# Performance work log

Hardware: AMD Instinct MI355X
Metric: run time of the kernel (lower is better)

## Reference

```python
import jax, jax.numpy as jnp
import numpy as np

N_NODES = 50000
N_EDGES = 1600000
IN_FEATS = 256
ENC_H = 20
DEC_H = 64
BIAS = 0.0  # forward arg default
TEMPERATURE = 1.0


def setup_inputs() -> dict:
    key = jax.random.key(0)
    ks = jax.random.split(key, 8)
    x = jax.random.normal(ks[0], (N_NODES, IN_FEATS), dtype=jnp.float32)
    edge_index = jax.random.randint(ks[1], (2, N_EDGES), 0, N_NODES, dtype=jnp.int64)
    node_id = 42
    # GCNConv params (glorot-ish scale)
    W_gcn = jax.random.normal(ks[2], (IN_FEATS, ENC_H), dtype=jnp.float32) / np.sqrt(IN_FEATS)
    b_gcn = jnp.zeros((ENC_H,), dtype=jnp.float32)
    # decoder MLP params
    W1 = jax.random.normal(ks[3], (3 * ENC_H, DEC_H), dtype=jnp.float32) / np.sqrt(3 * ENC_H)
    b1 = jnp.zeros((DEC_H,), dtype=jnp.float32)
    W2 = jax.random.normal(ks[4], (DEC_H, 1), dtype=jnp.float32) / np.sqrt(DEC_H)
    b2 = jnp.zeros((1,), dtype=jnp.float32)
    return {"x": x, "edge_index": edge_index, "node_id": node_id,
            "W_gcn": W_gcn, "b_gcn": b_gcn, "W1": W1, "b1": b1, "W2": W2, "b2": b2}


def _gcn_conv(x, edge_index, W, b):
    """PyG GCNConv: add self loops, symmetric normalization, sum aggregation."""
    n = x.shape[0]
    xw = x @ W  # [N, ENC_H]
    loop = jnp.arange(n, dtype=edge_index.dtype)
    row = jnp.concatenate([edge_index[0], loop])  # source
    col = jnp.concatenate([edge_index[1], loop])  # target
    ones = jnp.ones(row.shape[0], dtype=x.dtype)
    deg = jax.ops.segment_sum(ones, col, num_segments=n)
    dinv = jnp.where(deg > 0, jax.lax.rsqrt(jnp.maximum(deg, 1e-12)), 0.0)
    norm = dinv[row] * dinv[col]  # [E+N]
    msgs = xw[row] * norm[:, None]
    out = jax.ops.segment_sum(msgs, col, num_segments=n)
    return out + b


def reference(x, edge_index, node_id, W_gcn, b_gcn, W1, b1, W2, b2):
    # encoder: GCN + ReLU
    enc = jax.nn.relu(_gcn_conv(x, edge_index, W_gcn, b_gcn))  # [N, ENC_H]
    # edge representation: [row_embed | col_embed | node_embed]
    rows, cols = edge_index[0], edge_index[1]
    node_embed = jnp.broadcast_to(enc[node_id], (rows.shape[0], enc.shape[1]))
    z = jnp.concatenate([enc[rows], enc[cols], node_embed], axis=1)  # [E, 3*ENC_H]
    # decoder MLP
    h = jax.nn.relu(z @ W1 + b1)
    out_dec = h @ W2 + b2  # [E, 1]
    # Gumbel-sigmoid sampling (training=True path)
    bias = BIAS + 0.0001
    u = jax.random.uniform(jax.random.key(123), out_dec.shape, dtype=out_dec.dtype)
    eps = (bias - (1.0 - bias)) * u + (1.0 - bias)  # in (bias, 1-bias)
    gate = jnp.log(eps) - jnp.log1p(-eps)
    return jax.nn.sigmoid((gate + out_dec) / TEMPERATURE)
```

## Files before the change

kernel.cpp:

```cpp
#include <hip/hip_runtime.h>
#include <hip/hip_bf16.h>

#define IN_FEATS 256
#define ENC_H    20
#define DEC_H    64
#define EPB      8192

__device__ __forceinline__ unsigned int rotl32(unsigned int x, int d) {
  return (x << d) | (x >> (32 - d));
}

__device__ __forceinline__ void threefry2x32(unsigned int k0, unsigned int k1,
                                             unsigned int x0, unsigned int x1,
                                             unsigned int& o0, unsigned int& o1) {
  unsigned int ks0 = k0, ks1 = k1, ks2 = k0 ^ k1 ^ 0x1BD11BDAu;
  x0 += ks0; x1 += ks1;
  x0 += x1; x1 = rotl32(x1, 13); x1 ^= x0;
  x0 += x1; x1 = rotl32(x1, 15); x1 ^= x0;
  x0 += x1; x1 = rotl32(x1, 26); x1 ^= x0;
  x0 += x1; x1 = rotl32(x1,  6); x1 ^= x0;
  x0 += ks1; x1 += ks2 + 1u;
  x0 += x1; x1 = rotl32(x1, 17); x1 ^= x0;
  x0 += x1; x1 = rotl32(x1, 29); x1 ^= x0;
  x0 += x1; x1 = rotl32(x1, 16); x1 ^= x0;
  x0 += x1; x1 = rotl32(x1, 24); x1 ^= x0;
  x0 += ks2; x1 += ks0 + 2u;
  x0 += x1; x1 = rotl32(x1, 13); x1 ^= x0;
  x0 += x1; x1 = rotl32(x1, 15); x1 ^= x0;
  x0 += x1; x1 = rotl32(x1, 26); x1 ^= x0;
  x0 += x1; x1 = rotl32(x1,  6); x1 ^= x0;
  x0 += ks0; x1 += ks1 + 3u;
  x0 += x1; x1 = rotl32(x1, 17); x1 ^= x0;
  x0 += x1; x1 = rotl32(x1, 29); x1 ^= x0;
  x0 += x1; x1 = rotl32(x1, 16); x1 ^= x0;
  x0 += x1; x1 = rotl32(x1, 24); x1 ^= x0;
  x0 += ks1; x1 += ks2 + 4u;
  x0 += x1; x1 = rotl32(x1, 13); x1 ^= x0;
  x0 += x1; x1 = rotl32(x1, 15); x1 ^= x0;
  x0 += x1; x1 = rotl32(x1, 26); x1 ^= x0;
  x0 += x1; x1 = rotl32(x1,  6); x1 ^= x0;
  x0 += ks2; x1 += ks0 + 5u;
  o0 = x0; o1 = x1;
}

__device__ __forceinline__ float2 bf2_unpack(unsigned int u) {
  float2 f;
  f.x = __uint_as_float(u << 16);
  f.y = __uint_as_float(u & 0xffff0000u);
  return f;
}


__global__ __launch_bounds__(1024) void k_binhist(const int* __restrict__ col,
                                                  int* __restrict__ bbc, int E, int nbins) {
  __shared__ int h[256];
  int t = threadIdx.x;
  if (t < 256) h[t] = 0;
  __syncthreads();
  int lo = blockIdx.x * EPB;
  int hi = min(lo + EPB, E);
  for (int e = lo + t; e < hi; e += 1024) atomicAdd(&h[col[e] >> 8], 1);
  __syncthreads();
  if (t < nbins) bbc[blockIdx.x * nbins + t] = h[t];
}

__global__ void k_colA(const int* __restrict__ bbc, int* __restrict__ base,
                       int* __restrict__ binTot, int nblk, int nbins) {
  __shared__ int sd[256];
  int t = threadIdx.x;
  int bin = blockIdx.x;
  int v = (t < nblk) ? bbc[(size_t)t * nbins + bin] : 0;
  sd[t] = v;
  __syncthreads();
#pragma unroll
  for (int off = 1; off < 256; off <<= 1) {
    int tmp = (t >= off) ? sd[t - off] : 0;
    __syncthreads();
    sd[t] += tmp;
    __syncthreads();
  }
  if (t < nblk) base[(size_t)t * nbins + bin] = sd[t] - v;
  if (t == 255) binTot[bin] = sd[255];
}

__global__ void k_colB(const int* __restrict__ binTot, int* __restrict__ binStart, int nbins) {
  __shared__ int sd[256];
  int t = threadIdx.x;
  int v = (t < nbins) ? binTot[t] : 0;
  sd[t] = v;
  __syncthreads();
#pragma unroll
  for (int off = 1; off < 256; off <<= 1) {
    int tmp = (t >= off) ? sd[t - off] : 0;
    __syncthreads();
    sd[t] += tmp;
    __syncthreads();
  }
  if (t < nbins) {
    binStart[t] = sd[t] - v;
    if (t == nbins - 1) binStart[nbins] = sd[t];
  }
}

__global__ __launch_bounds__(1024) void k_binscatter(const int* __restrict__ row,
                                                     const int* __restrict__ col,
                                                     const int* __restrict__ base,
                                                     const int* __restrict__ binStart,
                                                     unsigned long long* __restrict__ binned,
                                                     int E, int nbins) {
  __shared__ int cur[256];
  int t = threadIdx.x;
  if (t < nbins) cur[t] = binStart[t] + base[(size_t)blockIdx.x * nbins + t];
  __syncthreads();
  int lo = blockIdx.x * EPB;
  int hi = min(lo + EPB, E);
  for (int e = lo + t; e < hi; e += 1024) {
    int c = col[e];
    int slot = atomicAdd(&cur[c >> 8], 1);
    binned[slot] = (unsigned long long)(unsigned int)row[e]
                 | ((unsigned long long)(unsigned int)c << 16)
                 | ((unsigned long long)(unsigned int)e << 32);
  }
}

__global__ __launch_bounds__(1024) void k_binsort(const unsigned long long* __restrict__ binned,
                                                  const int* __restrict__ binStart,
                                                  unsigned long long* __restrict__ sorted,
                                                  int* __restrict__ nstart,
                                                  float* __restrict__ dinv,
                                                  int N, int E) {
  __shared__ int cnt[256];
  __shared__ int ls[256];
  __shared__ int cur[256];
  int t = threadIdx.x;
  int bin = blockIdx.x;
  if (t < 256) cnt[t] = 0;
  __syncthreads();
  int s = binStart[bin], epos = binStart[bin + 1];
  const unsigned int* b32 = (const unsigned int*)binned;
  for (int i = s + t; i < epos; i += 1024)
    atomicAdd(&cnt[(b32[2 * (size_t)i] >> 16) & 0xFFu], 1);
  __syncthreads();
  int v = (t < 256) ? cnt[t] : 0;
  if (t < 256) ls[t] = v;
  __syncthreads();
#pragma unroll
  for (int off = 1; off < 256; off <<= 1) {
    int tmp = 0;
    if (t < 256 && t >= off) tmp = ls[t - off];
    __syncthreads();
    if (t < 256 && t >= off) ls[t] += tmp;
    __syncthreads();
  }
  if (t < 256) {
    int ex = ls[t] - v;
    cur[t] = s + ex;
    int n = (bin << 8) + t;
    if (n < N) {
      nstart[n] = s + ex;
      dinv[n] = rsqrtf((float)(v + 1));
    }
  }
  if (bin == 0 && t == 0) nstart[N] = E;
  __syncthreads();
  for (int i = s + t; i < epos; i += 1024) {
    unsigned long long e64 = binned[i];
    int cl = (int)((e64 >> 16) & 0xFFu);
    int slot = atomicAdd(&cur[cl], 1);
    sorted[slot] = e64;
  }
}


__global__ void k_xw(const float* __restrict__ x, const float* __restrict__ W,
                     const float* __restrict__ dinv, __hip_bfloat16* __restrict__ xwd, int N) {
  __shared__ float Wl[IN_FEATS * ENC_H];
  for (int i = threadIdx.x; i < IN_FEATS * ENC_H; i += blockDim.x) Wl[i] = W[i];
  __syncthreads();
  int g = blockIdx.x * blockDim.x + threadIdx.x;
  int n = g >> 2, part = g & 3;
  if (n >= N) return;
  float acc[ENC_H];
#pragma unroll
  for (int j = 0; j < ENC_H; j++) acc[j] = 0.0f;
  const float4* x4 = reinterpret_cast<const float4*>(x + (size_t)n * IN_FEATS);
#pragma unroll 4
  for (int k4 = 0; k4 < 16; k4++) {
    float4 v = x4[k4 * 4 + part];
    int kbase = k4 * 16 + part * 4;
    const float* w0 = &Wl[(kbase + 0) * ENC_H];
    const float* w1 = &Wl[(kbase + 1) * ENC_H];
    const float* w2 = &Wl[(kbase + 2) * ENC_H];
    const float* w3 = &Wl[(kbase + 3) * ENC_H];
#pragma unroll
    for (int j = 0; j < ENC_H; j++) {
      acc[j] = fmaf(v.x, w0[j], acc[j]);
      acc[j] = fmaf(v.y, w1[j], acc[j]);
      acc[j] = fmaf(v.z, w2[j], acc[j]);
      acc[j] = fmaf(v.w, w3[j], acc[j]);
    }
  }
#pragma unroll
  for (int j = 0; j < ENC_H; j++) acc[j] += __shfl_xor(acc[j], 1);
#pragma unroll
  for (int j = 0; j < ENC_H; j++) acc[j] += __shfl_xor(acc[j], 2);
  float d = dinv[n];
  __hip_bfloat16* o = xwd + (size_t)n * ENC_H;
  int jb = part * 5;
#pragma unroll
  for (int jj = 0; jj < 5; jj++) o[jb + jj] = __float2bfloat16(acc[jb + jj] * d);
}

__global__ void k_gather(const int* __restrict__ nstart,
                         const unsigned long long* __restrict__ sorted,
                         const __hip_bfloat16* __restrict__ xwd, const float* __restrict__ dinv,
                         const float* __restrict__ bg, float* __restrict__ enc, int N) {
  int t = blockIdx.x * blockDim.x + threadIdx.x;
  int n = t / ENC_H;
  int j = t % ENC_H;
  if (n >= N) return;
  int s = nstart[n], epos = nstart[n + 1];
  float acc = __bfloat162float(xwd[(size_t)n * ENC_H + j]);
  const unsigned int* b32 = (const unsigned int*)sorted;
  for (int k = s; k < epos; k++) {
    int r = (int)(b32[2 * (size_t)k] & 0xFFFFu);
    acc += __bfloat162float(xwd[(size_t)r * ENC_H + j]);
  }
  float v = acc * dinv[n] + bg[j];
  enc[(size_t)n * ENC_H + j] = fmaxf(v, 0.0f);
}

__global__ void k_pq(const float* __restrict__ enc, const float* __restrict__ W1,
                     __hip_bfloat16* __restrict__ P1, __hip_bfloat16* __restrict__ P2,
                     __hip_bfloat16* __restrict__ Q1, __hip_bfloat16* __restrict__ Q2, int N) {
  __shared__ float Wl[2 * ENC_H * DEC_H];
  for (int i = threadIdx.x; i < 2 * ENC_H * DEC_H; i += blockDim.x) Wl[i] = W1[i];
  __syncthreads();
  int t = blockIdx.x * blockDim.x + threadIdx.x;
  int n = t / DEC_H, j = t % DEC_H;
  if (n >= N) return;
  const float* en = enc + (size_t)n * ENC_H;
  float p = 0.0f, q = 0.0f;
#pragma unroll
  for (int k = 0; k < ENC_H; k++) {
    float ev = en[k];
    p = fmaf(ev, Wl[k * DEC_H + j], p);
    q = fmaf(ev, Wl[(k + ENC_H) * DEC_H + j], q);
  }
  size_t idx = (size_t)n * 32 + (j & 31);
  if (j < 32) { P1[idx] = __float2bfloat16(p); Q1[idx] = __float2bfloat16(q); }
  else        { P2[idx] = __float2bfloat16(p); Q2[idx] = __float2bfloat16(q); }
}

__global__ void k_t3(const float* __restrict__ enc, const float* __restrict__ W1,
                     const float* __restrict__ b1, const int* __restrict__ node_id,
                     float* __restrict__ t3) {
  int j = threadIdx.x;
  int nid = node_id[0];
  const float* en = enc + (size_t)nid * ENC_H;
  float a = b1[j];
#pragma unroll
  for (int k = 0; k < ENC_H; k++) a = fmaf(en[k], W1[(2 * ENC_H + k) * DEC_H + j], a);
  t3[j] = a;
}

template <int HALF>
__global__ void k_dec_half(const unsigned long long* __restrict__ sorted,
                           const __hip_bfloat16* __restrict__ Ph,
                           const __hip_bfloat16* __restrict__ Qh,
                           const float* __restrict__ t3, const float* __restrict__ W2,
                           const float* __restrict__ b2,
                           float* __restrict__ partial, float* __restrict__ out, int E) {
  __shared__ float t3l[32], w2l[32];
  if (threadIdx.x < 32) {
    t3l[threadIdx.x] = t3[HALF * 32 + threadIdx.x];
    w2l[threadIdx.x] = W2[HALF * 32 + threadIdx.x];
  }
  __syncthreads();
  int pos = blockIdx.x * blockDim.x + threadIdx.x;
  if (pos >= E) return;
  unsigned long long v = sorted[pos];
  int r = (int)(v & 0xFFFFu);
  int c = (int)((v >> 16) & 0xFFFFu);
  const uint4* pr = reinterpret_cast<const uint4*>(Ph + (size_t)r * 32);
  const uint4* qc = reinterpret_cast<const uint4*>(Qh + (size_t)c * 32);
  float acc = 0.0f;
#pragma unroll
  for (int b = 0; b < 4; b++) {
    uint4 pu = pr[b];
    uint4 qu = qc[b];
    int j0 = b * 8;
    float2 p0 = bf2_unpack(pu.x), q0 = bf2_unpack(qu.x);
    float2 p1 = bf2_unpack(pu.y), q1 = bf2_unpack(qu.y);
    float2 p2 = bf2_unpack(pu.z), q2 = bf2_unpack(qu.z);
    float2 p3 = bf2_unpack(pu.w), q3 = bf2_unpack(qu.w);
    float h;
    h = fmaxf(p0.x + q0.x + t3l[j0 + 0], 0.0f); acc = fmaf(h, w2l[j0 + 0], acc);
    h = fmaxf(p0.y + q0.y + t3l[j0 + 1], 0.0f); acc = fmaf(h, w2l[j0 + 1], acc);
    h = fmaxf(p1.x + q1.x + t3l[j0 + 2], 0.0f); acc = fmaf(h, w2l[j0 + 2], acc);
    h = fmaxf(p1.y + q1.y + t3l[j0 + 3], 0.0f); acc = fmaf(h, w2l[j0 + 3], acc);
    h = fmaxf(p2.x + q2.x + t3l[j0 + 4], 0.0f); acc = fmaf(h, w2l[j0 + 4], acc);
    h = fmaxf(p2.y + q2.y + t3l[j0 + 5], 0.0f); acc = fmaf(h, w2l[j0 + 5], acc);
    h = fmaxf(p3.x + q3.x + t3l[j0 + 6], 0.0f); acc = fmaf(h, w2l[j0 + 6], acc);
    h = fmaxf(p3.y + q3.y + t3l[j0 + 7], 0.0f); acc = fmaf(h, w2l[j0 + 7], acc);
  }
  if (HALF == 0) {
    partial[pos] = acc;
  } else {
    unsigned int e = (unsigned int)(v >> 32);
    float od = acc + partial[pos] + b2[0];
    unsigned int o0, o1;
    threefry2x32(0u, 123u, 0u, e, o0, o1);
    unsigned int bits = o0 ^ o1;
    float u = __uint_as_float((bits >> 9) | 0x3f800000u) - 1.0f;
    float eps = (-0.9998f) * u + 0.9999f;
    float gate = logf(eps) - log1pf(-eps);
    float s = 1.0f / (1.0f + expf(-(gate + od)));
    out[e] = s;
  }
}

extern "C" void kernel_launch(void* const* d_in, const int* in_sizes, int n_in,
                              void* d_out, int out_size, void* d_ws, size_t ws_size,
                              hipStream_t stream) {
  const float* x       = (const float*)d_in[0];
  const int*   edge    = (const int*)d_in[1];
  const int*   node_id = (const int*)d_in[2];
  const float* W_gcn   = (const float*)d_in[3];
  const float* b_gcn   = (const float*)d_in[4];
  const float* W1      = (const float*)d_in[5];
  const float* b1      = (const float*)d_in[6];
  const float* W2      = (const float*)d_in[7];
  const float* b2      = (const float*)d_in[8];
  float* out = (float*)d_out;

  int N = in_sizes[0] / IN_FEATS;
  int E = in_sizes[1] / 2;
  const int* erow = edge;
  const int* ecol = edge + E;
  int nbins = (N + 255) >> 8;
  int NB = (E + EPB - 1) / EPB;

  char* ws = (char*)d_ws;
  size_t off = 0;
  auto alloc = [&](size_t bytes) {
    char* p = ws + off;
    off = (off + bytes + 255) & ~(size_t)255;
    return p;
  };
  __hip_bfloat16* xwd = (__hip_bfloat16*)alloc((size_t)N * ENC_H * sizeof(__hip_bfloat16));
  float* enc  = (float*)alloc((size_t)N * ENC_H * sizeof(float));
  float* dinv = (float*)alloc((size_t)N * sizeof(float));
  int*  nstart = (int*)alloc((size_t)(N + 1) * sizeof(int));
  unsigned long long* binned = (unsigned long long*)alloc((size_t)E * sizeof(unsigned long long));
  unsigned long long* sorted = (unsigned long long*)alloc((size_t)E * sizeof(unsigned long long));
  int* bbc      = (int*)alloc((size_t)NB * nbins * sizeof(int));
  int* base     = (int*)alloc((size_t)NB * nbins * sizeof(int));
  int* binTot   = (int*)alloc((size_t)nbins * sizeof(int));
  int* binStart = (int*)alloc((size_t)(nbins + 1) * sizeof(int));
  __hip_bfloat16* P1 = (__hip_bfloat16*)alloc((size_t)N * 32 * sizeof(__hip_bfloat16));
  __hip_bfloat16* P2 = (__hip_bfloat16*)alloc((size_t)N * 32 * sizeof(__hip_bfloat16));
  __hip_bfloat16* Q1 = (__hip_bfloat16*)alloc((size_t)N * 32 * sizeof(__hip_bfloat16));
  __hip_bfloat16* Q2 = (__hip_bfloat16*)alloc((size_t)N * 32 * sizeof(__hip_bfloat16));
  float* partial = (float*)alloc((size_t)E * sizeof(float));
  float* t3   = (float*)alloc((size_t)DEC_H * sizeof(float));
  (void)ws_size; (void)n_in; (void)out_size;

  const int B = 256;
  int ge  = (E + B - 1) / B;
  int gxw = (N * 4 + B - 1) / B;
  int gg  = (N * ENC_H + B - 1) / B;
  int gpq = (N * DEC_H + B - 1) / B;

  k_binhist   <<<NB, 1024, 0, stream>>>(ecol, bbc, E, nbins);
  k_colA      <<<nbins, 256, 0, stream>>>(bbc, base, binTot, NB, nbins);
  k_colB      <<<1, 256, 0, stream>>>(binTot, binStart, nbins);
  k_binscatter<<<NB, 1024, 0, stream>>>(erow, ecol, base, binStart, binned, E, nbins);
  k_binsort   <<<nbins, 1024, 0, stream>>>(binned, binStart, sorted, nstart, dinv, N, E);
  k_xw        <<<gxw, B, 0, stream>>>(x, W_gcn, dinv, xwd, N);
  k_gather    <<<gg, B, 0, stream>>>(nstart, sorted, xwd, dinv, b_gcn, enc, N);
  k_pq        <<<gpq, B, 0, stream>>>(enc, W1, P1, P2, Q1, Q2, N);
  k_t3        <<<1, DEC_H, 0, stream>>>(enc, W1, b1, node_id, t3);
  k_dec_half<0><<<ge, B, 0, stream>>>(sorted, P1, Q1, t3, W2, b2, partial, out, E);
  k_dec_half<1><<<ge, B, 0, stream>>>(sorted, P2, Q2, t3, W2, b2, partial, out, E);
}
```

Baseline: 186.3 us.

## Shrink edge records and move output scatter into a separate final kernel

Binned edges shrink from 64-bit to 32-bit packed row/col, and the fully sorted array keeps only a 16-bit row index for the gather. The decoder now reads edges in bin order and writes partial sums in that order. A new final kernel maps each original edge through an inverse-permutation array, computes the Gumbel-sigmoid and writes coalesced output. This cuts the bytes moved for edge records and replaces scattered output writes with gathered reads, at the cost of an extra einv array, one more launch and another pass over partial.

Result: no change. 187.5 us (+0.6%).

```diff
diff --git a/kernel.cpp b/kernel.cpp
--- a/kernel.cpp
+++ b/kernel.cpp
@@ -106,7 +106,8 @@
                                                      const int* __restrict__ col,
                                                      const int* __restrict__ base,
                                                      const int* __restrict__ binStart,
-                                                     unsigned long long* __restrict__ binned,
+                                                     unsigned int* __restrict__ binned,
+                                                     int* __restrict__ einv,
                                                      int E, int nbins) {
   __shared__ int cur[256];
   int t = threadIdx.x;
@@ -117,15 +118,14 @@
   for (int e = lo + t; e < hi; e += 1024) {
     int c = col[e];
     int slot = atomicAdd(&cur[c >> 8], 1);
-    binned[slot] = (unsigned long long)(unsigned int)row[e]
-                 | ((unsigned long long)(unsigned int)c << 16)
-                 | ((unsigned long long)(unsigned int)e << 32);
-  }
-}
-
-__global__ __launch_bounds__(1024) void k_binsort(const unsigned long long* __restrict__ binned,
+    binned[slot] = (unsigned int)row[e] | ((unsigned int)c << 16);
+    einv[e] = slot;
+  }
+}
+
+__global__ __launch_bounds__(1024) void k_binsort(const unsigned int* __restrict__ binned,
                                                   const int* __restrict__ binStart,
-                                                  unsigned long long* __restrict__ sorted,
+                                                  unsigned short* __restrict__ sorted_r,
                                                   int* __restrict__ nstart,
                                                   float* __restrict__ dinv,
                                                   int N, int E) {
@@ -137,9 +137,8 @@
   if (t < 256) cnt[t] = 0;
   __syncthreads();
   int s = binStart[bin], epos = binStart[bin + 1];
-  const unsigned int* b32 = (const unsigned int*)binned;
   for (int i = s + t; i < epos; i += 1024)
-    atomicAdd(&cnt[(b32[2 * (size_t)i] >> 16) & 0xFFu], 1);
+    atomicAdd(&cnt[(binned[i] >> 16) & 0xFFu], 1);
   __syncthreads();
   int v = (t < 256) ? cnt[t] : 0;
   if (t < 256) ls[t] = v;
@@ -164,10 +163,10 @@
   if (bin == 0 && t == 0) nstart[N] = E;
   __syncthreads();
   for (int i = s + t; i < epos; i += 1024) {
-    unsigned long long e64 = binned[i];
-    int cl = (int)((e64 >> 16) & 0xFFu);
+    unsigned int e32 = binned[i];
+    int cl = (int)((e32 >> 16) & 0xFFu);
     int slot = atomicAdd(&cur[cl], 1);
-    sorted[slot] = e64;
+    sorted_r[slot] = (unsigned short)(e32 & 0xFFFFu);
   }
 }
 
@@ -212,7 +211,7 @@
 }
 
 __global__ void k_gather(const int* __restrict__ nstart,
-                         const unsigned long long* __restrict__ sorted,
+                         const unsigned short* __restrict__ sorted_r,
                          const __hip_bfloat16* __restrict__ xwd, const float* __restrict__ dinv,
                          const float* __restrict__ bg, float* __restrict__ enc, int N) {
   int t = blockIdx.x * blockDim.x + threadIdx.x;
@@ -221,9 +220,8 @@
   if (n >= N) return;
   int s = nstart[n], epos = nstart[n + 1];
   float acc = __bfloat162float(xwd[(size_t)n * ENC_H + j]);
-  const unsigned int* b32 = (const unsigned int*)sorted;
   for (int k = s; k < epos; k++) {
-    int r = (int)(b32[2 * (size_t)k] & 0xFFFFu);
+    int r = (int)sorted_r[k];
     acc += __bfloat162float(xwd[(size_t)r * ENC_H + j]);
   }
   float v = acc * dinv[n] + bg[j];
@@ -265,12 +263,12 @@
 }
 
 template <int HALF>
-__global__ void k_dec_half(const unsigned long long* __restrict__ sorted,
+__global__ void k_dec_half(const unsigned int* __restrict__ binned,
                            const __hip_bfloat16* __restrict__ Ph,
                            const __hip_bfloat16* __restrict__ Qh,
                            const float* __restrict__ t3, const float* __restrict__ W2,
                            const float* __restrict__ b2,
-                           float* __restrict__ partial, float* __restrict__ out, int E) {
+                           float* __restrict__ partial, int E) {
   __shared__ float t3l[32], w2l[32];
   if (threadIdx.x < 32) {
     t3l[threadIdx.x] = t3[HALF * 32 + threadIdx.x];
@@ -279,9 +277,9 @@
   __syncthreads();
   int pos = blockIdx.x * blockDim.x + threadIdx.x;
   if (pos >= E) return;
-  unsigned long long v = sorted[pos];
+  unsigned int v = binned[pos];
   int r = (int)(v & 0xFFFFu);
-  int c = (int)((v >> 16) & 0xFFFFu);
+  int c = (int)(v >> 16);
   const uint4* pr = reinterpret_cast<const uint4*>(Ph + (size_t)r * 32);
   const uint4* qc = reinterpret_cast<const uint4*>(Qh + (size_t)c * 32);
   float acc = 0.0f;
@@ -307,17 +305,23 @@
   if (HALF == 0) {
     partial[pos] = acc;
   } else {
-    unsigned int e = (unsigned int)(v >> 32);
-    float od = acc + partial[pos] + b2[0];
-    unsigned int o0, o1;
-    threefry2x32(0u, 123u, 0u, e, o0, o1);
-    unsigned int bits = o0 ^ o1;
-    float u = __uint_as_float((bits >> 9) | 0x3f800000u) - 1.0f;
-    float eps = (-0.9998f) * u + 0.9999f;
-    float gate = logf(eps) - log1pf(-eps);
-    float s = 1.0f / (1.0f + expf(-(gate + od)));
-    out[e] = s;
-  }
+    partial[pos] += acc + b2[0];
+  }
+}
+
+__global__ void k_final(const int* __restrict__ einv, const float* __restrict__ partial,
+                        float* __restrict__ out, int E) {
+  int e = blockIdx.x * blockDim.x + threadIdx.x;
+  if (e >= E) return;
+  float od = partial[einv[e]];
+  unsigned int o0, o1;
+  threefry2x32(0u, 123u, 0u, (unsigned int)e, o0, o1);
+  unsigned int bits = o0 ^ o1;
+  float u = __uint_as_float((bits >> 9) | 0x3f800000u) - 1.0f;
+  float eps = (-0.9998f) * u + 0.9999f;
+  float gate = logf(eps) - log1pf(-eps);
+  float s = 1.0f / (1.0f + expf(-(gate + od)));
+  out[e] = s;
 }
 
 extern "C" void kernel_launch(void* const* d_in, const int* in_sizes, int n_in,
@@ -352,8 +356,9 @@
   float* enc  = (float*)alloc((size_t)N * ENC_H * sizeof(float));
   float* dinv = (float*)alloc((size_t)N * sizeof(float));
   int*  nstart = (int*)alloc((size_t)(N + 1) * sizeof(int));
-  unsigned long long* binned = (unsigned long long*)alloc((size_t)E * sizeof(unsigned long long));
-  unsigned long long* sorted = (unsigned long long*)alloc((size_t)E * sizeof(unsigned long long));
+  unsigned int*   binned   = (unsigned int*)alloc((size_t)E * sizeof(unsigned int));
+  int*            einv     = (int*)alloc((size_t)E * sizeof(int));
+  unsigned short* sorted_r = (unsigned short*)alloc((size_t)E * sizeof(unsigned short));
   int* bbc      = (int*)alloc((size_t)NB * nbins * sizeof(int));
   int* base     = (int*)alloc((size_t)NB * nbins * sizeof(int));
   int* binTot   = (int*)alloc((size_t)nbins * sizeof(int));
@@ -375,12 +380,13 @@
   k_binhist   <<<NB, 1024, 0, stream>>>(ecol, bbc, E, nbins);
   k_colA      <<<nbins, 256, 0, stream>>>(bbc, base, binTot, NB, nbins);
   k_colB      <<<1, 256, 0, stream>>>(binTot, binStart, nbins);
-  k_binscatter<<<NB, 1024, 0, stream>>>(erow, ecol, base, binStart, binned, E, nbins);
-  k_binsort   <<<nbins, 1024, 0, stream>>>(binned, binStart, sorted, nstart, dinv, N, E);
+  k_binscatter<<<NB, 1024, 0, stream>>>(erow, ecol, base, binStart, binned, einv, E, nbins);
+  k_binsort   <<<nbins, 1024, 0, stream>>>(binned, binStart, sorted_r, nstart, dinv, N, E);
   k_xw        <<<gxw, B, 0, stream>>>(x, W_gcn, dinv, xwd, N);
-  k_gather    <<<gg, B, 0, stream>>>(nstart, sorted, xwd, dinv, b_gcn, enc, N);
+  k_gather    <<<gg, B, 0, stream>>>(nstart, sorted_r, xwd, dinv, b_gcn, enc, N);
   k_pq        <<<gpq, B, 0, stream>>>(enc, W1, P1, P2, Q1, Q2, N);
   k_t3        <<<1, DEC_H, 0, stream>>>(enc, W1, b1, node_id, t3);
-  k_dec_half<0><<<ge, B, 0, stream>>>(sorted, P1, Q1, t3, W2, b2, partial, out, E);
-  k_dec_half<1><<<ge, B, 0, stream>>>(sorted, P2, Q2, t3, W2, b2, partial, out, E);
-}
+  k_dec_half<0><<<ge, B, 0, stream>>>(binned, P1, Q1, t3, W2, b2, partial, E);
+  k_dec_half<1><<<ge, B, 0, stream>>>(binned, P2, Q2, t3, W2, b2, partial, E);
+  k_final     <<<ge, B, 0, stream>>>(einv, partial, out, E);
+}
```
